# Kernel tuning notes

Measured on AMD Instinct MI355X. Metric: run time of the kernel, lower is better.

Reference implementation:

```python
import jax, jax.numpy as jnp
import numpy as np

B = 524288      # batch
CONT = 64       # continuous features
N_CATE = 16     # categorical fields
VOCAB = 1000    # vocab per field
EM = 8          # embedding dim
LOW = EM * N_CATE + CONT  # 192
R = 32          # representation dim
RH = 32         # rep hidden dim
PH = 16         # head hidden dim
N_HEAD = 8      # number of routing heads


def setup_inputs() -> dict:
    key = jax.random.key(0)
    ks = jax.random.split(key, 16)
    s = 0.05
    return {
        "x_cont": jax.random.normal(ks[0], (B, CONT), dtype=jnp.float32),
        "x_cate": jax.random.randint(ks[1], (B, N_CATE), 0, VOCAB, dtype=jnp.int64),
        "t": jax.random.randint(ks[2], (B, 1), 0, N_HEAD, dtype=jnp.int64),
        # embedding tables, one per categorical field
        "emb": jax.random.normal(ks[3], (N_CATE, VOCAB, EM), dtype=jnp.float32) * s,
        # representation DNN: LOW -> RH -> RH -> R (2 hidden layers + output)
        "W1": jax.random.normal(ks[4], (LOW, RH), dtype=jnp.float32) * s,
        "b1": jnp.zeros((RH,), dtype=jnp.float32),
        "W2": jax.random.normal(ks[5], (RH, RH), dtype=jnp.float32) * s,
        "b2": jnp.zeros((RH,), dtype=jnp.float32),
        "W3": jax.random.normal(ks[6], (RH, R), dtype=jnp.float32) * s,
        "b3": jnp.zeros((R,), dtype=jnp.float32),
        # stacked per-head DNNs: R -> PH -> 1 (1 hidden layer + output)
        "HW1": jax.random.normal(ks[7], (N_HEAD, R, PH), dtype=jnp.float32) * s,
        "Hb1": jnp.zeros((N_HEAD, PH), dtype=jnp.float32),
        "HW2": jax.random.normal(ks[8], (N_HEAD, PH, 1), dtype=jnp.float32) * s,
        "Hb2": jnp.zeros((N_HEAD, 1), dtype=jnp.float32),
    }


def reference(x_cont, x_cate, t, emb, W1, b1, W2, b2, W3, b3, HW1, Hb1, HW2, Hb2):
    # LowFeature: embed each categorical field and concat with continuous
    # emb[f, x_cate[:, f]] -> [B, N_CATE, EM]
    e = emb[jnp.arange(N_CATE)[None, :], x_cate]
    x = jnp.concatenate([x_cont, e.reshape(e.shape[0], -1)], axis=1)  # [B, LOW]
    # representation DNN (eval mode: dropout is identity)
    h = jax.nn.relu(x @ W1 + b1)
    h = jax.nn.relu(h @ W2 + b2)
    r = h @ W3 + b3  # [B, R]
    # evaluate all heads batched, then gather the routed head per sample
    hh = jax.nn.relu(jnp.einsum('br,nrh->bnh', r, HW1) + Hb1[None])  # [B, N_HEAD, PH]
    y_all = jnp.einsum('bnh,nho->bno', hh, HW2) + Hb2[None]          # [B, N_HEAD, 1]
    y = jnp.take_along_axis(y_all[..., 0], t, axis=1)[:, 0]          # [B]
    return y
```

## Files before the change

kernel.cpp:

```cpp
#include <hip/hip_runtime.h>

namespace {

typedef float  f32x4  __attribute__((ext_vector_type(4)));
typedef float  f32x16 __attribute__((ext_vector_type(16)));
typedef short  bf16x8 __attribute__((ext_vector_type(8)));
typedef int    i32x4  __attribute__((ext_vector_type(4)));
typedef unsigned int u32;

constexpr int kRows  = 524288;
constexpr int kCont  = 64;
constexpr int kNCate = 16;
constexpr int kVocab = 1000;
constexpr int kEm    = 8;
constexpr int kRH    = 32;
constexpr int kPH    = 16;

constexpr int    kNFrag = 48;
constexpr size_t kOffEH = (size_t)kNFrag * 1024;
constexpr size_t kOffHG = kOffEH + 256000;
constexpr size_t kOffHB = kOffHG + 16384;

__device__ inline u32 rne_hi(float x) {
    u32 u = __float_as_uint(x);
    return ((u + 0x7fffu + ((u >> 16) & 1u)) >> 16) & 0xffffu;
}
__device__ inline float hi_f32(u32 h) { return __uint_as_float(h << 16); }
__device__ inline u32 pack2(float a, float b) {
    return rne_hi(a) | (rne_hi(b) << 16);
}

union FragU { u32 w[4]; bf16x8 v; uint4 u4; };

__device__ inline f32x16 mfma16(bf16x8 a, bf16x8 b, f32x16 c) {
    return __builtin_amdgcn_mfma_f32_32x32x16_bf16(a, b, c, 0, 0, 0);
}
__device__ inline f32x16 zero16() {
    f32x16 z;
#pragma unroll
    for (int i = 0; i < 16; ++i) z[i] = 0.f;
    return z;
}
__device__ inline void gload_lds16(const void* g, void* l) {
    __builtin_amdgcn_global_load_lds(
        (const __attribute__((address_space(1))) void*)g,
        (__attribute__((address_space(3))) void*)l, 16, 0, 0);
}
__device__ inline void fence_vm0() {
    asm volatile("s_waitcnt vmcnt(0)" ::: "memory");
    __builtin_amdgcn_sched_barrier(0);
}
__device__ inline void fence_lgkm0() {
    asm volatile("s_waitcnt lgkmcnt(0)" ::: "memory");
    __builtin_amdgcn_sched_barrier(0);
}

__global__ __launch_bounds__(256) void build_hg(
    const float* __restrict__ W3, const float* __restrict__ HW1,
    const float* __restrict__ b3, const float* __restrict__ Hb1,
    float* __restrict__ HG, float* __restrict__ Hb1p)
{
    const int gid = blockIdx.x * blockDim.x + threadIdx.x;
    if (gid < 8 * 32 * 16) {
        const int n = gid >> 9, k = (gid >> 4) & 31, ph = gid & 15;
        const float* w3r = W3 + k * 32;
        const float* h1p = HW1 + (size_t)n * kRH * kPH + ph;
        float s = 0.f;
#pragma unroll
        for (int j = 0; j < 32; ++j) s = fmaf(w3r[j], h1p[j * kPH], s);
        HG[gid] = s;
    }
    if (gid < 128) {
        const int n = gid >> 4, ph = gid & 15;
        const float* h1p = HW1 + (size_t)n * kRH * kPH + ph;
        float s = Hb1[n * kPH + ph];
#pragma unroll
        for (int j = 0; j < 32; ++j) s = fmaf(b3[j], h1p[j * kPH], s);
        Hb1p[gid] = s;
    }
}

__global__ __launch_bounds__(256) void build_wfrags(
    const float* __restrict__ W1, const float* __restrict__ W2,
    const float* __restrict__ W3, const float* __restrict__ HG,
    ushort* __restrict__ WF)
{
    int gid = blockIdx.x * blockDim.x + threadIdx.x;
    if (gid >= kNFrag * 64) return;
    const int q = gid >> 6, l = gid & 63;
    const int lc = l & 31, g = l >> 5;

    const float* src; int k0, col, ldn, p;
    if (q < 12) {
        src = W1; col = lc; ldn = 32; p = 0;
        k0 = (q < 4) ? (16*q + 8*g) : (64 + 8*(q - 4) + 64*g);
    } else if (q < 24) {
        int f = q - 12;
        src = W1; col = lc; ldn = 32; p = 1;
        k0 = (f < 4) ? (16*f + 8*g) : (64 + 8*(f - 4) + 64*g);
    }
    else if (q < 28) { int u2 = q-24; src = W2; k0 = 16*(u2>>1) + 8*g; col = lc; ldn = 32; p = u2&1; }
    else if (q < 32) { int u2 = q-28; src = W3; k0 = 16*(u2>>1) + 8*g; col = lc; ldn = 32; p = u2&1; }
    else {
        int u2 = q-32; int n = u2>>2; int f = (u2>>1)&1; p = u2&1;
        int c128 = n*32 + lc; int head = c128 >> 4, ph = c128 & 15;
        src = HG + (size_t)head * kRH * kPH + ph;
        k0 = 16*f + 8*g; col = 0; ldn = kPH;
    }

    u32 hv[8];
#pragma unroll
    for (int j = 0; j < 8; ++j) {
        float w = src[(size_t)(k0 + j) * ldn + col];
        u32 h = rne_hi(w);
        hv[j] = (p == 0) ? h : rne_hi(w - hi_f32(h));
    }
    FragU fu;
#pragma unroll
    for (int w = 0; w < 4; ++w) fu.w[w] = hv[2*w] | (hv[2*w+1] << 16);
    ((uint4*)WF)[q * 64 + l] = fu.u4;
}

__global__ __launch_bounds__(256) void build_embhi(
    const float* __restrict__ emb, ushort* __restrict__ eh)
{
    int r = blockIdx.x * blockDim.x + threadIdx.x;
    if (r >= kNCate * kVocab) return;
    const float* e = emb + (size_t)r * kEm;
    FragU H;
#pragma unroll
    for (int w = 0; w < 4; ++w)
        H.w[w] = pack2(e[2*w], e[2*w+1]);
    ((uint4*)eh)[r] = H.u4;
}

__device__ inline void transition(const float* v, int g, FragU* H, FragU* L) {
    u32 hw[8], lw[8];
#pragma unroll
    for (int p = 0; p < 8; ++p) {
        float v0 = v[2*p], v1 = v[2*p+1];
        u32 h0 = rne_hi(v0), h1 = rne_hi(v1);
        hw[p] = h0 | (h1 << 16);
        lw[p] = pack2(v0 - hi_f32(h0), v1 - hi_f32(h1));
    }
#pragma unroll
    for (int f2 = 0; f2 < 2; ++f2) {
        u32 hp[4], lp[4];
#pragma unroll
        for (int p = 0; p < 4; ++p) {
            hp[p] = (u32)__shfl_xor((int)hw[4*f2 + p], 32);
            lp[p] = (u32)__shfl_xor((int)lw[4*f2 + p], 32);
        }
        H[f2].w[0] = g ? hp[2] : hw[4*f2+0];
        H[f2].w[1] = g ? hp[3] : hw[4*f2+1];
        H[f2].w[2] = g ? hw[4*f2+2] : hp[0];
        H[f2].w[3] = g ? hw[4*f2+3] : hp[1];
        L[f2].w[0] = g ? lp[2] : lw[4*f2+0];
        L[f2].w[1] = g ? lp[3] : lw[4*f2+1];
        L[f2].w[2] = g ? lw[4*f2+2] : lp[0];
        L[f2].w[3] = g ? lw[4*f2+3] : lp[1];
    }
}

__global__ __launch_bounds__(256, 3) void fused_main(
    const float* __restrict__ xc, const int* __restrict__ xcate,
    const int* __restrict__ tptr,
    const ushort* __restrict__ WF,
    const ushort* __restrict__ eh,
    const float* __restrict__ b1, const float* __restrict__ b2,
    const float* __restrict__ Hb1p,
    const float* __restrict__ HW2, const float* __restrict__ Hb2,
    float* __restrict__ out)
{
    __shared__ __align__(16) uint4 sW4[16 * 64];
    __shared__ __align__(16) float sX[4][2048];
    __shared__ __align__(16) float sB[328];

    const int tid = threadIdx.x;
    const uint4* wf4 = (const uint4*)WF;

#pragma unroll
    for (int it = 0; it < 4; ++it) {
        const int i = tid + 256 * it;
        sW4[i] = wf4[i];
    }
    for (int i = tid; i < 328; i += 256) {
        float v;
        if      (i < 32)  v = b1[i];
        else if (i < 64)  v = b2[i - 32];
        else if (i < 192) v = Hb1p[i - 64];
        else if (i < 320) v = HW2[i - 192];
        else              v = Hb2[i - 320];
        sB[i] = v;
    }
    __syncthreads();

    const int wv = tid >> 6, l = tid & 63;
    const int lc = l & 31, g = l >> 5;
    const int rowbase = blockIdx.x * 256 + wv * 64;
    char* xb = (char*)&sX[wv][0];
    const uint4* eh4 = (const uint4*)eh;

    auto stage_x = [&](int tbase) {
        const float* xbase = xc + (size_t)tbase * kCont;
#pragma unroll
        for (int i = 0; i < 8; ++i) {
            const int r   = 4*i + (l >> 4);
            const int c4s = (l & 15) ^ (r & 15);
            gload_lds16(xbase + r * kCont + c4s * 4, xb + i * 1024);
        }
    };
    auto load_idx = [&](int tbase, i32x4* iq, int& t_lane) {
        const i32x4* cr4 = (const i32x4*)(xcate + (size_t)(tbase + lc) * kNCate + 8*g);
        iq[0] = cr4[0];
        iq[1] = cr4[1];
        t_lane = tptr[tbase + lc];
    };
    auto gather_emb = [&](const i32x4* iq, uint4* ehv) {
#pragma unroll
        for (int i = 0; i < 8; ++i) {
            const int c   = i + 8*g;
            const int idx = (i < 4) ? iq[0][i] : iq[1][i - 4];
            ehv[i] = eh4[(size_t)(c * kVocab + idx)];
        }
    };
    auto layer1_cont = [&](f32x16& acca, f32x16& accb) {
#pragma unroll
        for (int f = 0; f < 4; ++f) {
            const int c0 = 4*f + 2*g;
            f32x4 va0 = *(const f32x4*)(xb + lc*256 + (((c0)     ^ (lc & 15)) * 16));
            f32x4 va1 = *(const f32x4*)(xb + lc*256 + (((c0 + 1) ^ (lc & 15)) * 16));
            FragU H, L;
#pragma unroll
            for (int w = 0; w < 4; ++w) {
                const f32x4& va = (w < 2) ? va0 : va1;
                const float v0 = va[2*(w & 1)], v1 = va[2*(w & 1) + 1];
                u32 h0 = rne_hi(v0), h1 = rne_hi(v1);
                H.w[w] = h0 | (h1 << 16);
                L.w[w] = pack2(v0 - hi_f32(h0), v1 - hi_f32(h1));
            }
            FragU WH, WL;
            WH.u4 = sW4[f * 64 + l];
            WL.u4 = sW4[(12 + f) * 64 + l];
            f32x16& acc = (f & 1) ? accb : acca;
            acc = mfma16(WH.v, H.v, acc);
            acc = mfma16(WL.v, H.v, acc);
            acc = mfma16(WH.v, L.v, acc);
        }
    };
    auto layer1_emb = [&](const uint4* ehv, f32x16& acca, f32x16& accb) {
#pragma unroll
        for (int i = 0; i < 8; ++i) {
            const int f = 4 + i;
            FragU BH, WH;
            BH.u4 = ehv[i];
            WH.u4 = sW4[f * 64 + l];
            f32x16& acc = (f & 1) ? accb : acca;
            acc = mfma16(WH.v, BH.v, acc);
        }
    };
    auto mid = [&](const f32x16& acca, const f32x16& accb, FragU* aHh, FragU* aHl) {
        float v1v[16];
#pragma unroll
        for (int p = 0; p < 4; ++p) {
            f32x4 bq = *(const f32x4*)&sB[0 + 8*p + 4*g];
#pragma unroll
            for (int m = 0; m < 4; ++m)
                v1v[4*p + m] = fmaxf(acca[4*p + m] + accb[4*p + m] + bq[m], 0.f);
        }
        FragU a2h[2], a2l[2];
        transition(v1v, g, a2h, a2l);

        f32x16 acc2 = zero16();
#pragma unroll
        for (int f2 = 0; f2 < 2; ++f2) {
            FragU WH, WL;
            WH.u4 = wf4[(24 + 2*f2) * 64 + l];
            WL.u4 = wf4[(25 + 2*f2) * 64 + l];
            acc2 = mfma16(WH.v, a2h[f2].v, acc2);
            acc2 = mfma16(WL.v, a2h[f2].v, acc2);
            acc2 = mfma16(WH.v, a2l[f2].v, acc2);
        }
        float v2v[16];
#pragma unroll
        for (int p = 0; p < 4; ++p) {
            f32x4 bq = *(const f32x4*)&sB[32 + 8*p + 4*g];
#pragma unroll
            for (int m = 0; m < 4; ++m)
                v2v[4*p + m] = fmaxf(acc2[4*p + m] + bq[m], 0.f);
        }
        transition(v2v, g, aHh, aHl);
    };
    auto heads_store = [&](const FragU* aHh, const FragU* aHl, int t_lane, int arow) {
        const f32x4 hb1q0 = *(const f32x4*)&sB[64  + t_lane*16 + 4*g];
        const f32x4 hb1q1 = *(const f32x4*)&sB[64  + t_lane*16 + 8 + 4*g];
        const f32x4 hw2q0 = *(const f32x4*)&sB[192 + t_lane*16 + 4*g];
        const f32x4 hw2q1 = *(const f32x4*)&sB[192 + t_lane*16 + 8 + 4*g];

        float ys = 0.f;
#pragma unroll
        for (int n = 0; n < 4; ++n) {
            f32x16 hacc = zero16();
#pragma unroll
            for (int f2 = 0; f2 < 2; ++f2) {
                FragU WH, WL;
                WH.u4 = wf4[(32 + 4*n + 2*f2) * 64 + l];
                WL.u4 = wf4[(33 + 4*n + 2*f2) * 64 + l];
                hacc = mfma16(WH.v, aHh[f2].v, hacc);
                hacc = mfma16(WL.v, aHh[f2].v, hacc);
                hacc = mfma16(WH.v, aHl[f2].v, hacc);
            }
            const bool sel = ((t_lane >> 1) == n);
            const bool half = (t_lane & 1);
#pragma unroll
            for (int j = 0; j < 8; ++j) {
                const float bb = (j < 4) ? hb1q0[j] : hb1q1[j - 4];
                const float ww = (j < 4) ? hw2q0[j] : hw2q1[j - 4];
                const float c0 = fmaxf(hacc[j]     + bb, 0.f) * ww;
                const float c1 = fmaxf(hacc[8 + j] + bb, 0.f) * ww;
                const float pick = half ? c1 : c0;
                ys += sel ? pick : 0.f;
            }
        }
        const float ytot = ys + __shfl_xor(ys, 32);
        if (g == 0)
            out[arow] = ytot + sB[320 + t_lane];
    };

    const int tb1 = rowbase, tb2 = rowbase + 32;

    stage_x(tb1);
    i32x4 iq1[2]; int t1;
    load_idx(tb1, iq1, t1);

    fence_vm0();

    uint4 ehv1[8];
    gather_emb(iq1, ehv1);

    f32x16 acca = zero16(), accb = zero16();
    layer1_cont(acca, accb);

    fence_lgkm0();
    stage_x(tb2);
    i32x4 iq2[2]; int t2;
    load_idx(tb2, iq2, t2);

    layer1_emb(ehv1, acca, accb);
    FragU aHh[2], aHl[2];
    mid(acca, accb, aHh, aHl);

    uint4 ehv2[8];
    gather_emb(iq2, ehv2);

    heads_store(aHh, aHl, t1, tb1 + lc);

    fence_vm0();

    acca = zero16(); accb = zero16();
    layer1_cont(acca, accb);
    layer1_emb(ehv2, acca, accb);
    mid(acca, accb, aHh, aHl);
    heads_store(aHh, aHl, t2, tb2 + lc);
}

}

extern "C" void kernel_launch(void* const* d_in, const int* in_sizes, int n_in,
                              void* d_out, int out_size, void* d_ws, size_t ws_size,
                              hipStream_t stream)
{
    const float* x_cont = (const float*)d_in[0];
    const int*   x_cate = (const int*)  d_in[1];
    const int*   t      = (const int*)  d_in[2];
    const float* emb    = (const float*)d_in[3];
    const float* W1     = (const float*)d_in[4];
    const float* b1     = (const float*)d_in[5];
    const float* W2     = (const float*)d_in[6];
    const float* b2     = (const float*)d_in[7];
    const float* W3     = (const float*)d_in[8];
    const float* b3     = (const float*)d_in[9];
    const float* HW1    = (const float*)d_in[10];
    const float* Hb1    = (const float*)d_in[11];
    const float* HW2    = (const float*)d_in[12];
    const float* Hb2    = (const float*)d_in[13];
    float* out = (float*)d_out;

    ushort* WF   = (ushort*)d_ws;
    ushort* eh   = (ushort*)((char*)d_ws + kOffEH);
    float*  HG   = (float*) ((char*)d_ws + kOffHG);
    float*  Hb1p = (float*) ((char*)d_ws + kOffHB);

    hipLaunchKernelGGL(build_hg, dim3(16), dim3(256), 0, stream,
                       W3, HW1, b3, Hb1, HG, Hb1p);
    hipLaunchKernelGGL(build_wfrags, dim3(12), dim3(256), 0, stream,
                       W1, W2, W3, HG, WF);
    hipLaunchKernelGGL(build_embhi, dim3((kNCate*kVocab + 255)/256), dim3(256), 0, stream,
                       emb, eh);

    const int grid = kRows / 256;
    hipLaunchKernelGGL(fused_main, dim3(grid), dim3(256), 0, stream,
                       x_cont, x_cate, t, WF, eh,
                       b1, b2, Hb1p, HW2, Hb2, out);
}
```

Baseline: 75.20 us.

## Interleave both 32-row tiles through all layers and load second tile into registers

Replaces the sequential two-tile software pipeline with a fully interleaved schedule. Both tiles' indices, embeddings and continuous features are loaded up front, the second tile going straight into registers instead of through LDS. Their MFMA chains then alternate so two independent accumulator chains hide MFMA latency. This raises register pressure, so the occupancy hint drops from 3 to 2 blocks per CU, which may reduce latency hiding for the gather loads.

```diff
diff --git a/kernel.cpp b/kernel.cpp
--- a/kernel.cpp
+++ b/kernel.cpp
@@ -48,10 +48,6 @@
 }
 __device__ inline void fence_vm0() {
     asm volatile("s_waitcnt vmcnt(0)" ::: "memory");
-    __builtin_amdgcn_sched_barrier(0);
-}
-__device__ inline void fence_lgkm0() {
-    asm volatile("s_waitcnt lgkmcnt(0)" ::: "memory");
     __builtin_amdgcn_sched_barrier(0);
 }
 
@@ -162,7 +158,7 @@
     }
 }
 
-__global__ __launch_bounds__(256, 3) void fused_main(
+__global__ __launch_bounds__(256, 2) void fused_main(
     const float* __restrict__ xc, const int* __restrict__ xcate,
     const int* __restrict__ tptr,
     const ushort* __restrict__ WF,
@@ -198,35 +194,58 @@
     const int wv = tid >> 6, l = tid & 63;
     const int lc = l & 31, g = l >> 5;
     const int rowbase = blockIdx.x * 256 + wv * 64;
+    const int tb1 = rowbase, tb2 = rowbase + 32;
     char* xb = (char*)&sX[wv][0];
     const uint4* eh4 = (const uint4*)eh;
 
-    auto stage_x = [&](int tbase) {
-        const float* xbase = xc + (size_t)tbase * kCont;
+    {
+        const float* xbase = xc + (size_t)tb1 * kCont;
 #pragma unroll
         for (int i = 0; i < 8; ++i) {
             const int r   = 4*i + (l >> 4);
             const int c4s = (l & 15) ^ (r & 15);
             gload_lds16(xbase + r * kCont + c4s * 4, xb + i * 1024);
         }
-    };
-    auto load_idx = [&](int tbase, i32x4* iq, int& t_lane) {
-        const i32x4* cr4 = (const i32x4*)(xcate + (size_t)(tbase + lc) * kNCate + 8*g);
-        iq[0] = cr4[0];
-        iq[1] = cr4[1];
-        t_lane = tptr[tbase + lc];
-    };
-    auto gather_emb = [&](const i32x4* iq, uint4* ehv) {
-#pragma unroll
-        for (int i = 0; i < 8; ++i) {
-            const int c   = i + 8*g;
-            const int idx = (i < 4) ? iq[0][i] : iq[1][i - 4];
-            ehv[i] = eh4[(size_t)(c * kVocab + idx)];
-        }
-    };
-    auto layer1_cont = [&](f32x16& acca, f32x16& accb) {
+    }
+    i32x4 iq1[2], iq2[2];
+    int t1, t2;
+    {
+        const i32x4* cr1 = (const i32x4*)(xcate + (size_t)(tb1 + lc) * kNCate + 8*g);
+        iq1[0] = cr1[0]; iq1[1] = cr1[1];
+        const i32x4* cr2 = (const i32x4*)(xcate + (size_t)(tb2 + lc) * kNCate + 8*g);
+        iq2[0] = cr2[0]; iq2[1] = cr2[1];
+        t1 = tptr[tb1 + lc];
+        t2 = tptr[tb2 + lc];
+    }
+    f32x4 xa2[8];
+    {
+        const f32x4* xr4 = (const f32x4*)(xc + (size_t)(tb2 + lc) * kCont);
 #pragma unroll
         for (int f = 0; f < 4; ++f) {
+            xa2[2*f]   = xr4[4*f + 2*g];
+            xa2[2*f+1] = xr4[4*f + 2*g + 1];
+        }
+    }
+
+    fence_vm0();
+
+    uint4 ehv1[8], ehv2[8];
+#pragma unroll
+    for (int i = 0; i < 8; ++i) {
+        const int c = i + 8*g;
+        const int i1 = (i < 4) ? iq1[0][i] : iq1[1][i - 4];
+        const int i2 = (i < 4) ? iq2[0][i] : iq2[1][i - 4];
+        ehv1[i] = eh4[(size_t)(c * kVocab + i1)];
+        ehv2[i] = eh4[(size_t)(c * kVocab + i2)];
+    }
+
+    f32x16 A1a = zero16(), A1b = zero16(), A2a = zero16(), A2b = zero16();
+#pragma unroll
+    for (int f = 0; f < 4; ++f) {
+        FragU WH, WL;
+        WH.u4 = sW4[f * 64 + l];
+        WL.u4 = sW4[(12 + f) * 64 + l];
+        {
             const int c0 = 4*f + 2*g;
             f32x4 va0 = *(const f32x4*)(xb + lc*256 + (((c0)     ^ (lc & 15)) * 16));
             f32x4 va1 = *(const f32x4*)(xb + lc*256 + (((c0 + 1) ^ (lc & 15)) * 16));
@@ -239,129 +258,137 @@
                 H.w[w] = h0 | (h1 << 16);
                 L.w[w] = pack2(v0 - hi_f32(h0), v1 - hi_f32(h1));
             }
-            FragU WH, WL;
-            WH.u4 = sW4[f * 64 + l];
-            WL.u4 = sW4[(12 + f) * 64 + l];
-            f32x16& acc = (f & 1) ? accb : acca;
+            f32x16& acc = (f & 1) ? A1b : A1a;
             acc = mfma16(WH.v, H.v, acc);
             acc = mfma16(WL.v, H.v, acc);
             acc = mfma16(WH.v, L.v, acc);
         }
-    };
-    auto layer1_emb = [&](const uint4* ehv, f32x16& acca, f32x16& accb) {
-#pragma unroll
-        for (int i = 0; i < 8; ++i) {
-            const int f = 4 + i;
-            FragU BH, WH;
-            BH.u4 = ehv[i];
-            WH.u4 = sW4[f * 64 + l];
-            f32x16& acc = (f & 1) ? accb : acca;
-            acc = mfma16(WH.v, BH.v, acc);
-        }
-    };
-    auto mid = [&](const f32x16& acca, const f32x16& accb, FragU* aHh, FragU* aHl) {
-        float v1v[16];
-#pragma unroll
-        for (int p = 0; p < 4; ++p) {
-            f32x4 bq = *(const f32x4*)&sB[0 + 8*p + 4*g];
-#pragma unroll
-            for (int m = 0; m < 4; ++m)
-                v1v[4*p + m] = fmaxf(acca[4*p + m] + accb[4*p + m] + bq[m], 0.f);
-        }
-        FragU a2h[2], a2l[2];
-        transition(v1v, g, a2h, a2l);
-
-        f32x16 acc2 = zero16();
-#pragma unroll
-        for (int f2 = 0; f2 < 2; ++f2) {
-            FragU WH, WL;
-            WH.u4 = wf4[(24 + 2*f2) * 64 + l];
-            WL.u4 = wf4[(25 + 2*f2) * 64 + l];
-            acc2 = mfma16(WH.v, a2h[f2].v, acc2);
-            acc2 = mfma16(WL.v, a2h[f2].v, acc2);
-            acc2 = mfma16(WH.v, a2l[f2].v, acc2);
-        }
-        float v2v[16];
-#pragma unroll
-        for (int p = 0; p < 4; ++p) {
-            f32x4 bq = *(const f32x4*)&sB[32 + 8*p + 4*g];
-#pragma unroll
-            for (int m = 0; m < 4; ++m)
-                v2v[4*p + m] = fmaxf(acc2[4*p + m] + bq[m], 0.f);
-        }
-        transition(v2v, g, aHh, aHl);
-    };
-    auto heads_store = [&](const FragU* aHh, const FragU* aHl, int t_lane, int arow) {
-        const f32x4 hb1q0 = *(const f32x4*)&sB[64  + t_lane*16 + 4*g];
-        const f32x4 hb1q1 = *(const f32x4*)&sB[64  + t_lane*16 + 8 + 4*g];
-        const f32x4 hw2q0 = *(const f32x4*)&sB[192 + t_lane*16 + 4*g];
-        const f32x4 hw2q1 = *(const f32x4*)&sB[192 + t_lane*16 + 8 + 4*g];
-
-        float ys = 0.f;
-#pragma unroll
-        for (int n = 0; n < 4; ++n) {
-            f32x16 hacc = zero16();
-#pragma unroll
-            for (int f2 = 0; f2 < 2; ++f2) {
-                FragU WH, WL;
-                WH.u4 = wf4[(32 + 4*n + 2*f2) * 64 + l];
-                WL.u4 = wf4[(33 + 4*n + 2*f2) * 64 + l];
-                hacc = mfma16(WH.v, aHh[f2].v, hacc);
-                hacc = mfma16(WL.v, aHh[f2].v, hacc);
-                hacc = mfma16(WH.v, aHl[f2].v, hacc);
+        {
+            f32x4 va0 = xa2[2*f], va1 = xa2[2*f+1];
+            FragU H, L;
+#pragma unroll
+            for (int w = 0; w < 4; ++w) {
+                const f32x4& va = (w < 2) ? va0 : va1;
+                const float v0 = va[2*(w & 1)], v1 = va[2*(w & 1) + 1];
+                u32 h0 = rne_hi(v0), h1 = rne_hi(v1);
+                H.w[w] = h0 | (h1 << 16);
+                L.w[w] = pack2(v0 - hi_f32(h0), v1 - hi_f32(h1));
             }
-            const bool sel = ((t_lane >> 1) == n);
-            const bool half = (t_lane & 1);
-#pragma unroll
-            for (int j = 0; j < 8; ++j) {
-                const float bb = (j < 4) ? hb1q0[j] : hb1q1[j - 4];
-                const float ww = (j < 4) ? hw2q0[j] : hw2q1[j - 4];
-                const float c0 = fmaxf(hacc[j]     + bb, 0.f) * ww;
-                const float c1 = fmaxf(hacc[8 + j] + bb, 0.f) * ww;
-                const float pick = half ? c1 : c0;
-                ys += sel ? pick : 0.f;
-            }
-        }
-        const float ytot = ys + __shfl_xor(ys, 32);
-        if (g == 0)
-            out[arow] = ytot + sB[320 + t_lane];
-    };
-
-    const int tb1 = rowbase, tb2 = rowbase + 32;
-
-    stage_x(tb1);
-    i32x4 iq1[2]; int t1;
-    load_idx(tb1, iq1, t1);
-
-    fence_vm0();
-
-    uint4 ehv1[8];
-    gather_emb(iq1, ehv1);
-
-    f32x16 acca = zero16(), accb = zero16();
-    layer1_cont(acca, accb);
-
-    fence_lgkm0();
-    stage_x(tb2);
-    i32x4 iq2[2]; int t2;
-    load_idx(tb2, iq2, t2);
-
-    layer1_emb(ehv1, acca, accb);
-    FragU aHh[2], aHl[2];
-    mid(acca, accb, aHh, aHl);
-
-    uint4 ehv2[8];
-    gather_emb(iq2, ehv2);
-
-    heads_store(aHh, aHl, t1, tb1 + lc);
-
-    fence_vm0();
-
-    acca = zero16(); accb = zero16();
-    layer1_cont(acca, accb);
-    layer1_emb(ehv2, acca, accb);
-    mid(acca, accb, aHh, aHl);
-    heads_store(aHh, aHl, t2, tb2 + lc);
+            f32x16& acc = (f & 1) ? A2b : A2a;
+            acc = mfma16(WH.v, H.v, acc);
+            acc = mfma16(WL.v, H.v, acc);
+            acc = mfma16(WH.v, L.v, acc);
+        }
+    }
+
+#pragma unroll
+    for (int i = 0; i < 8; ++i) {
+        const int f = 4 + i;
+        FragU WH;
+        WH.u4 = sW4[f * 64 + l];
+        FragU B1, B2;
+        B1.u4 = ehv1[i]; B2.u4 = ehv2[i];
+        f32x16& a1 = (f & 1) ? A1b : A1a;
+        f32x16& a2 = (f & 1) ? A2b : A2a;
+        a1 = mfma16(WH.v, B1.v, a1);
+        a2 = mfma16(WH.v, B2.v, a2);
+    }
+
+    float v1v1[16], v1v2[16];
+#pragma unroll
+    for (int p = 0; p < 4; ++p) {
+        f32x4 bq = *(const f32x4*)&sB[0 + 8*p + 4*g];
+#pragma unroll
+        for (int m = 0; m < 4; ++m) {
+            v1v1[4*p + m] = fmaxf(A1a[4*p + m] + A1b[4*p + m] + bq[m], 0.f);
+            v1v2[4*p + m] = fmaxf(A2a[4*p + m] + A2b[4*p + m] + bq[m], 0.f);
+        }
+    }
+    FragU a2h1[2], a2l1[2], a2h2[2], a2l2[2];
+    transition(v1v1, g, a2h1, a2l1);
+    transition(v1v2, g, a2h2, a2l2);
+
+    f32x16 C1 = zero16(), C2 = zero16();
+#pragma unroll
+    for (int f2 = 0; f2 < 2; ++f2) {
+        FragU WH, WL;
+        WH.u4 = wf4[(24 + 2*f2) * 64 + l];
+        WL.u4 = wf4[(25 + 2*f2) * 64 + l];
+        C1 = mfma16(WH.v, a2h1[f2].v, C1);
+        C2 = mfma16(WH.v, a2h2[f2].v, C2);
+        C1 = mfma16(WL.v, a2h1[f2].v, C1);
+        C2 = mfma16(WL.v, a2h2[f2].v, C2);
+        C1 = mfma16(WH.v, a2l1[f2].v, C1);
+        C2 = mfma16(WH.v, a2l2[f2].v, C2);
+    }
+    float v2v1[16], v2v2[16];
+#pragma unroll
+    for (int p = 0; p < 4; ++p) {
+        f32x4 bq = *(const f32x4*)&sB[32 + 8*p + 4*g];
+#pragma unroll
+        for (int m = 0; m < 4; ++m) {
+            v2v1[4*p + m] = fmaxf(C1[4*p + m] + bq[m], 0.f);
+            v2v2[4*p + m] = fmaxf(C2[4*p + m] + bq[m], 0.f);
+        }
+    }
+    FragU aHh1[2], aHl1[2], aHh2[2], aHl2[2];
+    transition(v2v1, g, aHh1, aHl1);
+    transition(v2v2, g, aHh2, aHl2);
+
+    const f32x4 hb1q0_1 = *(const f32x4*)&sB[64  + t1*16 + 4*g];
+    const f32x4 hb1q1_1 = *(const f32x4*)&sB[64  + t1*16 + 8 + 4*g];
+    const f32x4 hw2q0_1 = *(const f32x4*)&sB[192 + t1*16 + 4*g];
+    const f32x4 hw2q1_1 = *(const f32x4*)&sB[192 + t1*16 + 8 + 4*g];
+    const f32x4 hb1q0_2 = *(const f32x4*)&sB[64  + t2*16 + 4*g];
+    const f32x4 hb1q1_2 = *(const f32x4*)&sB[64  + t2*16 + 8 + 4*g];
+    const f32x4 hw2q0_2 = *(const f32x4*)&sB[192 + t2*16 + 4*g];
+    const f32x4 hw2q1_2 = *(const f32x4*)&sB[192 + t2*16 + 8 + 4*g];
+
+    float ys1 = 0.f, ys2 = 0.f;
+    const bool half1 = (t1 & 1), half2 = (t2 & 1);
+#pragma unroll
+    for (int n = 0; n < 4; ++n) {
+        FragU WH0, WL0, WH1, WL1;
+        WH0.u4 = wf4[(32 + 4*n + 0) * 64 + l];
+        WL0.u4 = wf4[(33 + 4*n + 0) * 64 + l];
+        WH1.u4 = wf4[(32 + 4*n + 2) * 64 + l];
+        WL1.u4 = wf4[(33 + 4*n + 2) * 64 + l];
+
+        f32x16 h1acc = zero16(), h2acc = zero16();
+        h1acc = mfma16(WH0.v, aHh1[0].v, h1acc);
+        h2acc = mfma16(WH0.v, aHh2[0].v, h2acc);
+        h1acc = mfma16(WL0.v, aHh1[0].v, h1acc);
+        h2acc = mfma16(WL0.v, aHh2[0].v, h2acc);
+        h1acc = mfma16(WH0.v, aHl1[0].v, h1acc);
+        h2acc = mfma16(WH0.v, aHl2[0].v, h2acc);
+        h1acc = mfma16(WH1.v, aHh1[1].v, h1acc);
+        h2acc = mfma16(WH1.v, aHh2[1].v, h2acc);
+        h1acc = mfma16(WL1.v, aHh1[1].v, h1acc);
+        h2acc = mfma16(WL1.v, aHh2[1].v, h2acc);
+        h1acc = mfma16(WH1.v, aHl1[1].v, h1acc);
+        h2acc = mfma16(WH1.v, aHl2[1].v, h2acc);
+
+        const bool sel1 = ((t1 >> 1) == n);
+        const bool sel2 = ((t2 >> 1) == n);
+#pragma unroll
+        for (int j = 0; j < 8; ++j) {
+            const float bb1 = (j < 4) ? hb1q0_1[j] : hb1q1_1[j - 4];
+            const float ww1 = (j < 4) ? hw2q0_1[j] : hw2q1_1[j - 4];
+            const float hv1 = half1 ? h1acc[8 + j] : h1acc[j];
+            ys1 += sel1 ? fmaxf(hv1 + bb1, 0.f) * ww1 : 0.f;
+            const float bb2 = (j < 4) ? hb1q0_2[j] : hb1q1_2[j - 4];
+            const float ww2 = (j < 4) ? hw2q0_2[j] : hw2q1_2[j - 4];
+            const float hv2 = half2 ? h2acc[8 + j] : h2acc[j];
+            ys2 += sel2 ? fmaxf(hv2 + bb2, 0.f) * ww2 : 0.f;
+        }
+    }
+
+    const float yt1 = ys1 + __shfl_xor(ys1, 32);
+    const float yt2 = ys2 + __shfl_xor(ys2, 32);
+    if (g == 0) {
+        out[tb1 + lc] = yt1 + sB[320 + t1];
+        out[tb2 + lc] = yt2 + sB[320 + t2];
+    }
 }
 
 }
```

After: 102.7 us. 1.37x slower.
